# Optimization experiments

Hardware: AMD Instinct MI355X
Metric: run time of the kernel (lower is better)

The kernel has to match this reference:

```python
import jax, jax.numpy as jnp
import numpy as np

B, T, K, H = 4, 2048, 1024, 16
D = K // H

def setup_inputs() -> dict:
    key = jax.random.key(0)
    kx, kq, kk, kv = jax.random.split(key, 4)
    s = 1.0 / np.sqrt(K)
    return {
        "x": jax.random.normal(kx, (B, T, K), dtype=jnp.float32),
        "Wq": jax.random.normal(kq, (K, K), dtype=jnp.float32) * s,
        "Wk": jax.random.normal(kk, (K, K), dtype=jnp.float32) * s,
        "Wv": jax.random.normal(kv, (K, K), dtype=jnp.float32) * s,
    }

def reference(x, Wq, Wk, Wv):
    b, t, k = x.shape
    h, d = H, K // H
    # projections -> (b, h, t, d)
    q = (x @ Wq.T).reshape(b, t, h, d).transpose(0, 2, 1, 3)
    ke = (x @ Wk.T).reshape(b, t, h, d).transpose(0, 2, 1, 3)
    v = (x @ Wv.T).reshape(b, t, h, d).transpose(0, 2, 1, 3)
    scale = d ** (-0.25)  # applied to both q and k, as in the original
    scores = jnp.einsum('bhqd,bhkd->bhqk', q * scale, ke * scale)
    causal = jnp.triu(jnp.ones((t, t), dtype=bool), k=1)
    scores = jnp.where(causal, -jnp.inf, scores)
    attn = jax.nn.softmax(scores, axis=-1)
    out = jnp.einsum('bhqk,bhkd->bhqd', attn, v)
    return out.transpose(0, 2, 1, 3).reshape(b, t, k)
```

## Files before the change

### kernel.cpp

```cpp
#include <hip/hip_runtime.h>
#include <hip/hip_bf16.h>
#include <math.h>

#define B_   4
#define T_   2048
#define KDIM 1024
#define H_   16
#define D_   64
#define BH_  (B_*H_)
#define M_   (B_*T_)
#define NKT  (KDIM/64)

typedef __bf16 bf16;
typedef __bf16 bf16x8 __attribute__((ext_vector_type(8)));
typedef __bf16 bf16x4 __attribute__((ext_vector_type(4)));
typedef float  f32x4  __attribute__((ext_vector_type(4)));
typedef float  f32x16 __attribute__((ext_vector_type(16)));
typedef unsigned int u32;
typedef u32 u32x4 __attribute__((ext_vector_type(4)));

static __device__ __forceinline__ f32x4 mfma16(bf16x8 a, bf16x8 b, f32x4 c) {
    return __builtin_amdgcn_mfma_f32_16x16x32_bf16(a, b, c, 0, 0, 0);
}
static __device__ __forceinline__ f32x16 mfma32(bf16x8 a, bf16x8 b, f32x16 c) {
    return __builtin_amdgcn_mfma_f32_32x32x16_bf16(a, b, c, 0, 0, 0);
}
static __device__ __forceinline__ float exp2_fast(float x) {
    float r; asm("v_exp_f32 %0, %1" : "=v"(r) : "v"(x)); return r;
}

__global__ void cvt_all(const float* __restrict__ x,  const float* __restrict__ Wq,
                        const float* __restrict__ Wk, const float* __restrict__ Wv,
                        bf16* __restrict__ dst) {
    int i = blockIdx.x * blockDim.x + threadIdx.x;
    const int NX = M_*KDIM/4, NW = KDIM*KDIM/4;
    const float* src;
    int j;
    if (i < NX)                { src = x;  j = i; }
    else if (i < NX + NW)      { src = Wq; j = i - NX; }
    else if (i < NX + 2*NW)    { src = Wk; j = i - NX - NW; }
    else                       { src = Wv; j = i - NX - 2*NW; }
    float4 v = reinterpret_cast<const float4*>(src)[j];
    bf16x4 o;
    o.x = (bf16)v.x; o.y = (bf16)v.y; o.z = (bf16)v.z; o.w = (bf16)v.w;
    reinterpret_cast<bf16x4*>(dst)[i] = o;
}

__global__ __launch_bounds__(256) void proj_gemm_db(
    const bf16* __restrict__ xb, const bf16* __restrict__ Wflat,
    bf16* __restrict__ Qb, bf16* __restrict__ Kb, bf16* __restrict__ Vtb)
{
    __shared__ __align__(16) char As[2][16384];
    __shared__ __align__(16) char Bs[2][16384];

    const int tid  = threadIdx.x;
    const int wid  = tid >> 6;
    const int lane = tid & 63;
    const int l15  = lane & 15, l4 = lane >> 4;
    const int wr = wid >> 1, wc = wid & 1;

    const int orig = blockIdx.x;
    const int xcd  = orig & 7;
    const int idx  = orig >> 3;
    const int mblk = xcd * 8 + (idx & 7);
    const int nblk = idx >> 3;
    const int row0 = mblk * 128, col0 = nblk * 128;

    const bf16* aS[4]; const bf16* bS[4];
#pragma unroll
    for (int q = 0; q < 4; ++q) {
        int c   = q*256 + tid;
        int rr  = c >> 3;
        int cb  = (c & 7) * 16;
        int cbs = cb ^ ((rr & 7) << 4);
        aS[q] = xb    + (size_t)(row0 + rr)*KDIM + (cbs >> 1);
        bS[q] = Wflat + (size_t)(col0 + rr)*KDIM + (cbs >> 1);
    }

    auto stage = [&](int kt, int buf) {
        if (kt >= NKT) return;
        const int k0 = kt * 64;
#pragma unroll
        for (int q = 0; q < 4; ++q) {
            char* la = As[buf] + (q*256 + wid*64)*16;
            __builtin_amdgcn_global_load_lds(
                (const __attribute__((address_space(1))) void*)(aS[q] + k0),
                (__attribute__((address_space(3))) void*)la, 16, 0, 0);
        }
#pragma unroll
        for (int q = 0; q < 4; ++q) {
            char* lb = Bs[buf] + (q*256 + wid*64)*16;
            __builtin_amdgcn_global_load_lds(
                (const __attribute__((address_space(1))) void*)(bS[q] + k0),
                (__attribute__((address_space(3))) void*)lb, 16, 0, 0);
        }
    };

    f32x4 acc[4][4] = {};
    const int sw   = (l15 & 7) << 4;
    const int arow = (wr*64 + l15) * 128;
    const int brow = (wc*64 + l15) * 128;

    stage(0, 0);
    stage(1, 1);

    for (int t = 0; t < NKT; ++t) {
        const int bt = t & 1;
        if (t + 1 < NKT) {
            asm volatile("s_waitcnt vmcnt(8)" ::: "memory");
        } else {
            asm volatile("s_waitcnt vmcnt(0)" ::: "memory");
        }
        __builtin_amdgcn_sched_barrier(0);
        __builtin_amdgcn_s_barrier();
        __builtin_amdgcn_sched_barrier(0);

        const char* Ap = As[bt];
        const char* Bp = Bs[bt];
#pragma unroll
        for (int kk = 0; kk < 2; ++kk) {
            const int cbk = (kk*64 + l4*16) ^ sw;
            bf16x8 af[4], bfr[4];
#pragma unroll
            for (int m = 0; m < 4; ++m)
                af[m] = *reinterpret_cast<const bf16x8*>(Ap + arow + m*2048 + cbk);
#pragma unroll
            for (int n = 0; n < 4; ++n)
                bfr[n] = *reinterpret_cast<const bf16x8*>(Bp + brow + n*2048 + cbk);
            __builtin_amdgcn_s_setprio(1);
#pragma unroll
            for (int m = 0; m < 4; ++m)
#pragma unroll
                for (int n = 0; n < 4; ++n)
                    acc[m][n] = mfma16(af[m], bfr[n], acc[m][n]);
            __builtin_amdgcn_s_setprio(0);
        }

        if (t + 2 < NKT) {
            asm volatile("s_waitcnt lgkmcnt(0)" ::: "memory");
            __builtin_amdgcn_sched_barrier(0);
            __builtin_amdgcn_s_barrier();
            __builtin_amdgcn_sched_barrier(0);
            stage(t + 2, bt);
        }
    }

#pragma unroll
    for (int m = 0; m < 4; ++m)
#pragma unroll
        for (int n = 0; n < 4; ++n)
#pragma unroll
            for (int r = 0; r < 4; ++r) {
                int gi = row0 + wr*64 + m*16 + l4*4 + r;
                int gj = col0 + wc*64 + n*16 + l15;
                int wz  = gj >> 10;
                int gjw = gj & 1023;
                float v = acc[m][n][r];
                if (wz == 0) v *= 0.18033688011112042f;
                bf16 o = (bf16)v;
                int bb = gi >> 11, tt = gi & (T_-1);
                int hh = gjw >> 6, dd = gjw & (D_-1);
                size_t bh = (size_t)bb*H_ + hh;
                if (wz == 0)      Qb [(bh*T_ + tt)*D_ + dd] = o;
                else if (wz == 1) Kb [(bh*T_ + tt)*D_ + dd] = o;
                else              Vtb[(bh*D_ + dd)*T_ + tt] = o;
            }
}

__global__ __launch_bounds__(256) void flash_attn3(
    const bf16* __restrict__ Qb, const bf16* __restrict__ Kb,
    const bf16* __restrict__ Vtb, float* __restrict__ out)
{
    __shared__ __align__(16) char Ksm[8192];
    __shared__ __align__(16) char Vsm[8192];

    const int tid  = threadIdx.x;
    const int wid  = tid >> 6;
    const int lane = tid & 63;
    const int l31  = lane & 31;
    const int hi   = lane >> 5;

    const int orig = blockIdx.x;
    const int wg   = (orig & 7) * 128 + (orig >> 3);
    const int bh   = wg >> 4;
    const int qblk = (15 - (wg & 15)) * 128;
    const int q0   = qblk + wid * 32;
    const int q_abs = q0 + l31;

    const bf16* qp = Qb + ((size_t)bh*T_ + q_abs)*D_ + hi*8;
    bf16x8 qf[4];
#pragma unroll
    for (int j = 0; j < 4; ++j)
        qf[j] = *reinterpret_cast<const bf16x8*>(qp + j*16);

    const bf16* kbase = Kb  + (size_t)bh*T_*D_;
    const bf16* vbase = Vtb + (size_t)bh*D_*T_;

    f32x16 o0 = {}; f32x16 o1 = {};
    float lsum = 0.f;

    const int my_nt  = (q0 + 31) >> 6;
    const int blk_nt = qblk/64 + 1;
    const int tmaskb = q_abs - 4*hi;

    const int r0 = tid >> 3,          r1 = (tid + 256) >> 3;
    const int e0 = (tid & 7) * 8;
    const u32 lds0 = (u32)((r0*128 + e0*2) ^ ((r0 & 7) << 4));
    const u32 lds1 = (u32)((r1*128 + e0*2) ^ ((r1 & 7) << 4));

    u32x4 kr0, kr1, vr0, vr1;
    auto issue = [&](int nt) {
        kr0 = *reinterpret_cast<const u32x4*>(kbase + ((size_t)(nt*64 + r0))*D_ + e0);
        kr1 = *reinterpret_cast<const u32x4*>(kbase + ((size_t)(nt*64 + r1))*D_ + e0);
        vr0 = *reinterpret_cast<const u32x4*>(vbase + (size_t)r0*T_ + nt*64 + e0);
        vr1 = *reinterpret_cast<const u32x4*>(vbase + (size_t)r1*T_ + nt*64 + e0);
    };
    issue(0);

    auto subtile = [&](int s, int kvb_abs, bool maskit, bf16x8& pA, bf16x8& pB) {
        f32x16 sacc = {};
        const int row = s*32 + l31;
        const int swk = (row & 7) << 4;
#pragma unroll
        for (int j = 0; j < 4; ++j) {
            bf16x8 kf = *reinterpret_cast<const bf16x8*>(Ksm + ((row*128 + j*32 + hi*16) ^ swk));
            sacc = mfma32(kf, qf[j], sacc);
        }
        const int tlim = tmaskb - kvb_abs;
        float p[16];
#pragma unroll
        for (int r = 0; r < 16; ++r) {
            const int crow0 = (r & 3) + 8*(r >> 2);
            float sv = sacc[r];
            if (maskit) sv = (crow0 > tlim) ? -INFINITY : sv;
            p[r] = exp2_fast(sv);
        }
        {
            float a0 = p[0]+p[1],   a1 = p[2]+p[3],   a2 = p[4]+p[5],   a3 = p[6]+p[7];
            float a4 = p[8]+p[9],   a5 = p[10]+p[11], a6 = p[12]+p[13], a7 = p[14]+p[15];
            lsum += ((a0+a1) + (a2+a3)) + ((a4+a5) + (a6+a7));
        }
        u32 w[8];
#pragma unroll
        for (int i = 0; i < 8; ++i) {
            u32 wv;
            asm("v_cvt_pk_bf16_f32 %0, %1, %2" : "=v"(wv) : "v"(p[2*i]), "v"(p[2*i+1]));
            w[i] = wv;
        }
        u32 a0w = w[0], a2w = w[2];
        asm("v_permlane32_swap_b32 %0, %1" : "+v"(a0w), "+v"(a2w));
        u32 a1w = w[1], a3w = w[3];
        asm("v_permlane32_swap_b32 %0, %1" : "+v"(a1w), "+v"(a3w));
        u32 b0w = w[4], b2w = w[6];
        asm("v_permlane32_swap_b32 %0, %1" : "+v"(b0w), "+v"(b2w));
        u32 b1w = w[5], b3w = w[7];
        asm("v_permlane32_swap_b32 %0, %1" : "+v"(b1w), "+v"(b3w));
        u32x4 A0 = {a0w, a1w, a2w, a3w};
        u32x4 A1 = {b0w, b1w, b2w, b3w};
        pA = __builtin_bit_cast(bf16x8, A0);
        pB = __builtin_bit_cast(bf16x8, A1);
    };

    auto pv = [&](int ks, bf16x8 pf) {
        const int swv = (l31 & 7) << 4;
        const int colb = ks*32 + hi*16;
        bf16x8 v0 = *reinterpret_cast<const bf16x8*>(Vsm + ((l31*128 + colb) ^ swv));
        bf16x8 v1 = *reinterpret_cast<const bf16x8*>(Vsm + (((32 + l31)*128 + colb) ^ swv));
        o0 = mfma32(v0, pf, o0);
        o1 = mfma32(v1, pf, o1);
    };

    for (int nt = 0; nt <= blk_nt; ++nt) {
        __syncthreads();
        *reinterpret_cast<u32x4*>(Ksm + lds0) = kr0;
        *reinterpret_cast<u32x4*>(Ksm + lds1) = kr1;
        *reinterpret_cast<u32x4*>(Vsm + lds0) = vr0;
        *reinterpret_cast<u32x4*>(Vsm + lds1) = vr1;
        __syncthreads();
        if (nt < blk_nt) issue(nt + 1);

        if (nt <= my_nt) {
            const bool partial = (nt == my_nt);
            const int  nsub = (!partial || (q0 & 32)) ? 2 : 1;
            bf16x8 pA, pB;
            subtile(0, nt*64, partial, pA, pB);
            pv(0, pA);
            pv(1, pB);
            if (nsub == 2) {
                subtile(1, nt*64 + 32, partial, pA, pB);
                pv(2, pA);
                pv(3, pB);
            }
        }
    }

    lsum += __shfl_xor(lsum, 32);
    const float inv = 1.0f / lsum;
    const int bb = bh >> 4, hh = bh & 15;
    float* orow = out + ((size_t)bb*T_ + q_abs)*KDIM + hh*64 + hi*4;
#pragma unroll
    for (int g = 0; g < 4; ++g) {
        f32x4 v0, v1;
#pragma unroll
        for (int j = 0; j < 4; ++j) { v0[j] = o0[g*4+j]*inv; v1[j] = o1[g*4+j]*inv; }
        *reinterpret_cast<f32x4*>(orow + g*8)      = v0;
        *reinterpret_cast<f32x4*>(orow + 32 + g*8) = v1;
    }
}

extern "C" void kernel_launch(void* const* d_in, const int* in_sizes, int n_in,
                              void* d_out, int out_size, void* d_ws, size_t ws_size,
                              hipStream_t stream) {
    (void)in_sizes; (void)n_in; (void)out_size; (void)ws_size;
    const float* x  = (const float*)d_in[0];
    const float* Wq = (const float*)d_in[1];
    const float* Wk = (const float*)d_in[2];
    const float* Wv = (const float*)d_in[3];
    float* out = (float*)d_out;

    bf16* xb  = (bf16*)d_ws;
    bf16* Wb  = xb + (size_t)M_*KDIM;
    bf16* Qb  = Wb + (size_t)3*KDIM*KDIM;
    bf16* Kb  = Qb + (size_t)M_*KDIM;
    bf16* Vtb = Kb + (size_t)M_*KDIM;

    const int n4 = (M_*KDIM + 3*KDIM*KDIM) / 4;
    cvt_all<<<(n4 + 255)/256, 256, 0, stream>>>(x, Wq, Wk, Wv, xb);

    proj_gemm_db<<<dim3(1536), 256, 0, stream>>>(xb, Wb, Qb, Kb, Vtb);
    flash_attn3<<<dim3(BH_*16), 256, 0, stream>>>(Qb, Kb, Vtb, out);
}
```

Baseline: 155.1 us.

## Restructure projection GEMM to 256x128 tiles, 8 waves, triple-buffered interleaved loads

```diff
diff --git a/kernel.cpp b/kernel.cpp
--- a/kernel.cpp
+++ b/kernel.cpp
@@ -46,80 +46,82 @@
     reinterpret_cast<bf16x4*>(dst)[i] = o;
 }
 
-__global__ __launch_bounds__(256) void proj_gemm_db(
+__global__ __launch_bounds__(512) void proj_gemm8p2(
     const bf16* __restrict__ xb, const bf16* __restrict__ Wflat,
     bf16* __restrict__ Qb, bf16* __restrict__ Kb, bf16* __restrict__ Vtb)
 {
-    __shared__ __align__(16) char As[2][16384];
-    __shared__ __align__(16) char Bs[2][16384];
+    __shared__ __align__(16) char As[3][32768];
+    __shared__ __align__(16) char Bs[3][16384];
 
     const int tid  = threadIdx.x;
     const int wid  = tid >> 6;
     const int lane = tid & 63;
     const int l15  = lane & 15, l4 = lane >> 4;
-    const int wr = wid >> 1, wc = wid & 1;
+    const int wavem = wid >> 1, waven = wid & 1;
 
     const int orig = blockIdx.x;
     const int xcd  = orig & 7;
     const int idx  = orig >> 3;
-    const int mblk = xcd * 8 + (idx & 7);
-    const int nblk = idx >> 3;
-    const int row0 = mblk * 128, col0 = nblk * 128;
-
-    const bf16* aS[4]; const bf16* bS[4];
+    const int mblk = xcd * 4 + (idx & 3);
+    const int nblk = idx >> 2;
+    const int row0 = mblk * 256, col0 = nblk * 128;
+
+    const bf16* aS[4];
 #pragma unroll
     for (int q = 0; q < 4; ++q) {
-        int c   = q*256 + tid;
+        int c   = q*512 + tid;
         int rr  = c >> 3;
         int cb  = (c & 7) * 16;
         int cbs = cb ^ ((rr & 7) << 4);
-        aS[q] = xb    + (size_t)(row0 + rr)*KDIM + (cbs >> 1);
+        aS[q] = xb + (size_t)(row0 + rr)*KDIM + (cbs >> 1);
+    }
+    const bf16* bS[2];
+#pragma unroll
+    for (int q = 0; q < 2; ++q) {
+        int c   = q*512 + tid;
+        int rr  = c >> 3;
+        int cb  = (c & 7) * 16;
+        int cbs = cb ^ ((rr & 7) << 4);
         bS[q] = Wflat + (size_t)(col0 + rr)*KDIM + (cbs >> 1);
     }
 
-    auto stage = [&](int kt, int buf) {
-        if (kt >= NKT) return;
-        const int k0 = kt * 64;
-#pragma unroll
-        for (int q = 0; q < 4; ++q) {
-            char* la = As[buf] + (q*256 + wid*64)*16;
-            __builtin_amdgcn_global_load_lds(
-                (const __attribute__((address_space(1))) void*)(aS[q] + k0),
-                (__attribute__((address_space(3))) void*)la, 16, 0, 0);
-        }
-#pragma unroll
-        for (int q = 0; q < 4; ++q) {
-            char* lb = Bs[buf] + (q*256 + wid*64)*16;
-            __builtin_amdgcn_global_load_lds(
-                (const __attribute__((address_space(1))) void*)(bS[q] + k0),
-                (__attribute__((address_space(3))) void*)lb, 16, 0, 0);
-        }
+    auto stA = [&](int kt, int s, int q) {
+        char* d = As[s] + (q*512 + wid*64)*16;
+        __builtin_amdgcn_global_load_lds(
+            (const __attribute__((address_space(1))) void*)(aS[q] + kt*64),
+            (__attribute__((address_space(3))) void*)d, 16, 0, 0);
+    };
+    auto stB = [&](int kt, int s, int q) {
+        char* d = Bs[s] + (q*512 + wid*64)*16;
+        __builtin_amdgcn_global_load_lds(
+            (const __attribute__((address_space(1))) void*)(bS[q] + kt*64),
+            (__attribute__((address_space(3))) void*)d, 16, 0, 0);
     };
 
     f32x4 acc[4][4] = {};
     const int sw   = (l15 & 7) << 4;
-    const int arow = (wr*64 + l15) * 128;
-    const int brow = (wc*64 + l15) * 128;
-
-    stage(0, 0);
-    stage(1, 1);
-
+    const int arow = (wavem*64 + l15) * 128;
+    const int brow = (waven*64 + l15) * 128;
+
+#pragma unroll
+    for (int q = 0; q < 4; ++q) stA(0, 0, q);
+    stB(0, 0, 0); stB(0, 0, 1);
+#pragma unroll
+    for (int q = 0; q < 4; ++q) stA(1, 1, q);
+    stB(1, 1, 0); stB(1, 1, 1);
+    asm volatile("s_waitcnt vmcnt(6)" ::: "memory");
+    __builtin_amdgcn_sched_barrier(0);
+    __builtin_amdgcn_s_barrier();
+
+    int s = 0, s2 = 2;
+#pragma unroll 1
     for (int t = 0; t < NKT; ++t) {
-        const int bt = t & 1;
-        if (t + 1 < NKT) {
-            asm volatile("s_waitcnt vmcnt(8)" ::: "memory");
-        } else {
-            asm volatile("s_waitcnt vmcnt(0)" ::: "memory");
-        }
-        __builtin_amdgcn_sched_barrier(0);
-        __builtin_amdgcn_s_barrier();
-        __builtin_amdgcn_sched_barrier(0);
-
-        const char* Ap = As[bt];
-        const char* Bp = Bs[bt];
-#pragma unroll
-        for (int kk = 0; kk < 2; ++kk) {
-            const int cbk = (kk*64 + l4*16) ^ sw;
+        const char* Ap = As[s];
+        const char* Bp = Bs[s];
+        const bool st = (t + 2 < NKT);
+
+        {
+            const int cbk = (l4*16) ^ sw;
             bf16x8 af[4], bfr[4];
 #pragma unroll
             for (int m = 0; m < 4; ++m)
@@ -127,6 +129,11 @@
 #pragma unroll
             for (int n = 0; n < 4; ++n)
                 bfr[n] = *reinterpret_cast<const bf16x8*>(Bp + brow + n*2048 + cbk);
+            if (st) { stA(t+2, s2, 0); stA(t+2, s2, 1); stB(t+2, s2, 0); }
+            __builtin_amdgcn_s_barrier();
+            __builtin_amdgcn_sched_barrier(0);
+            asm volatile("s_waitcnt lgkmcnt(0)" ::: "memory");
+            __builtin_amdgcn_sched_barrier(0);
             __builtin_amdgcn_s_setprio(1);
 #pragma unroll
             for (int m = 0; m < 4; ++m)
@@ -134,15 +141,42 @@
                 for (int n = 0; n < 4; ++n)
                     acc[m][n] = mfma16(af[m], bfr[n], acc[m][n]);
             __builtin_amdgcn_s_setprio(0);
-        }
-
-        if (t + 2 < NKT) {
+            __builtin_amdgcn_s_barrier();
+            __builtin_amdgcn_sched_barrier(0);
+        }
+
+        {
+            const int cbk = (64 + l4*16) ^ sw;
+            bf16x8 af[4], bfr[4];
+#pragma unroll
+            for (int m = 0; m < 4; ++m)
+                af[m] = *reinterpret_cast<const bf16x8*>(Ap + arow + m*2048 + cbk);
+#pragma unroll
+            for (int n = 0; n < 4; ++n)
+                bfr[n] = *reinterpret_cast<const bf16x8*>(Bp + brow + n*2048 + cbk);
+            if (st) { stA(t+2, s2, 2); stA(t+2, s2, 3); stB(t+2, s2, 1); }
+            if (t + 1 < NKT) {
+                if (st) { asm volatile("s_waitcnt vmcnt(6)" ::: "memory"); }
+                else    { asm volatile("s_waitcnt vmcnt(0)" ::: "memory"); }
+                __builtin_amdgcn_sched_barrier(0);
+            }
+            __builtin_amdgcn_s_barrier();
+            __builtin_amdgcn_sched_barrier(0);
             asm volatile("s_waitcnt lgkmcnt(0)" ::: "memory");
             __builtin_amdgcn_sched_barrier(0);
+            __builtin_amdgcn_s_setprio(1);
+#pragma unroll
+            for (int m = 0; m < 4; ++m)
+#pragma unroll
+                for (int n = 0; n < 4; ++n)
+                    acc[m][n] = mfma16(af[m], bfr[n], acc[m][n]);
+            __builtin_amdgcn_s_setprio(0);
             __builtin_amdgcn_s_barrier();
             __builtin_amdgcn_sched_barrier(0);
-            stage(t + 2, bt);
-        }
+        }
+
+        s  = (s  == 2) ? 0 : s  + 1;
+        s2 = (s2 == 2) ? 0 : s2 + 1;
     }
 
 #pragma unroll
@@ -151,8 +185,8 @@
         for (int n = 0; n < 4; ++n)
 #pragma unroll
             for (int r = 0; r < 4; ++r) {
-                int gi = row0 + wr*64 + m*16 + l4*4 + r;
-                int gj = col0 + wc*64 + n*16 + l15;
+                int gi = row0 + wavem*64 + m*16 + l4*4 + r;
+                int gj = col0 + waven*64 + n*16 + l15;
                 int wz  = gj >> 10;
                 int gjw = gj & 1023;
                 float v = acc[m][n][r];
@@ -217,9 +251,9 @@
     };
     issue(0);
 
-    auto subtile = [&](int s, int kvb_abs, bool maskit, bf16x8& pA, bf16x8& pB) {
+    auto subtile = [&](int sk, int kvb_abs, bool maskit, bf16x8& pA, bf16x8& pB) {
         f32x16 sacc = {};
-        const int row = s*32 + l31;
+        const int row = sk*32 + l31;
         const int swk = (row & 7) << 4;
 #pragma unroll
         for (int j = 0; j < 4; ++j) {
@@ -327,6 +361,6 @@
     const int n4 = (M_*KDIM + 3*KDIM*KDIM) / 4;
     cvt_all<<<(n4 + 255)/256, 256, 0, stream>>>(x, Wq, Wk, Wv, xb);
 
-    proj_gemm_db<<<dim3(1536), 256, 0, stream>>>(xb, Wb, Qb, Kb, Vtb);
+    proj_gemm8p2<<<dim3(768), 512, 0, stream>>>(xb, Wb, Qb, Kb, Vtb);
     flash_attn3<<<dim3(BH_*16), 256, 0, stream>>>(Qb, Kb, Vtb, out);
 }
```

After: 157.3 us. No clear change (+1.4%).
